# Kernel tuning notes

Measured on AMD Instinct MI355X. Metric: run time of the kernel, lower is better.

## Reference

```python
import jax, jax.numpy as jnp
import numpy as np

E = 8        # n_experts
H = 1024     # hidden_size == input_size
M = 2048     # intermediate_size
K = 2        # topk
SE = 1       # share_expert
BSZ, SEQ = 2, 1024
W_SCALE = 0.02


def setup_inputs() -> dict:
    key = jax.random.key(0)
    ks = jax.random.split(key, 9)
    return {
        "x": jax.random.normal(ks[0], (BSZ, SEQ, H), jnp.float32),
        "gate_w": jax.random.normal(ks[1], (E, H), jnp.float32) * W_SCALE,
        "beta": jnp.zeros((E,), jnp.float32),
        "gate_proj_w": jax.random.normal(ks[2], (E, H, M), jnp.float32) * W_SCALE,
        "up_proj_w": jax.random.normal(ks[3], (E, H, M), jnp.float32) * W_SCALE,
        "down_proj_w": jax.random.normal(ks[4], (E, M, H), jnp.float32) * W_SCALE,
        "shared_gate_w": jax.random.normal(ks[5], (SE, H, M), jnp.float32) * W_SCALE,
        "shared_up_w": jax.random.normal(ks[6], (SE, H, M), jnp.float32) * W_SCALE,
        "shared_down_w": jax.random.normal(ks[7], (SE, M, H), jnp.float32) * W_SCALE,
    }


def reference(x, gate_w, beta, gate_proj_w, up_proj_w, down_proj_w,
              shared_gate_w, shared_up_w, shared_down_w):
    B0, S0, H0 = x.shape
    xt = x.reshape(-1, H0)                       # [B, H], B = B0*S0 tokens
    B = xt.shape[0]

    # --- routing: top-k on (logits + beta), gate prob = sigmoid(selected logits) ---
    logits = xt @ gate_w.T                       # [B, E]
    _, idx = jax.lax.top_k(logits + beta, K)     # [B, K] expert indices
    probs = jax.nn.sigmoid(jnp.take_along_axis(logits, idx, axis=-1))  # [B, K]

    # combine weights c[b, e]: scatter top-k probs (equivalent to index_add combine)
    c = jnp.zeros((B, E), xt.dtype).at[jnp.arange(B)[:, None], idx].add(probs)

    # --- per-expert SwiGLU over all tokens, then weighted combine by c ---
    g = jnp.einsum('bh,ehm->bem', xt, gate_proj_w)   # [B, E, M]
    u = jnp.einsum('bh,ehm->bem', xt, up_proj_w)     # [B, E, M]
    h = jax.nn.silu(g) * u                           # [B, E, M]
    eo = jnp.einsum('bem,emh->beh', h, down_proj_w)  # [B, E, H]
    combined = jnp.einsum('beh,be->bh', eo, c)       # [B, H]

    # --- shared expert(s): applied to every token, no gating ---
    sg = jnp.einsum('bh,ehm->bem', xt, shared_gate_w)
    su = jnp.einsum('bh,ehm->bem', xt, shared_up_w)
    sh = jax.nn.silu(sg) * su
    shared_out = jnp.einsum('bem,emh->beh', sh, shared_down_w).sum(axis=1)  # [B, H]

    return (combined + shared_out).reshape(B0, S0, H0)
```

## Files before the change

kernel.cpp:

```cpp
#include <hip/hip_runtime.h>

#define NE 8
#define HD 1024
#define MD 2048
#define NT 2048
#define NSH 4224

typedef __attribute__((ext_vector_type(8))) short s16x8;
typedef __attribute__((ext_vector_type(4))) float f32x4;
typedef __attribute__((ext_vector_type(8))) unsigned short u16x8;
typedef __attribute__((ext_vector_type(4))) unsigned short u16x4;

__device__ __forceinline__ unsigned short f2bf(float f) {
    union { float f; unsigned int i; } v; v.f = f;
    unsigned int u = v.i;
    return (unsigned short)((u + 0x7FFFu + ((u >> 16) & 1u)) >> 16);
}
__device__ __forceinline__ float bf2f(unsigned short u) {
    union { unsigned int i; float f; } v; v.i = ((unsigned int)u) << 16; return v.f;
}

__device__ __forceinline__ void gld16(const unsigned short* g, short* l) {
    __builtin_amdgcn_global_load_lds(
        (const __attribute__((address_space(1))) unsigned int*)g,
        (__attribute__((address_space(3))) unsigned int*)l,
        16, 0, 0);
}


__global__ __launch_bounds__(256) void k_cvt(
    const float* __restrict__ s, unsigned short* __restrict__ d, int n)
{
    int i = (blockIdx.x * 256 + threadIdx.x) * 4;
    int stride = gridDim.x * 256 * 4;
    for (; i < n; i += stride) {
        float4 v = *(const float4*)(s + i);
        u16x4 o;
        o[0] = f2bf(v.x); o[1] = f2bf(v.y); o[2] = f2bf(v.z); o[3] = f2bf(v.w);
        *(u16x4*)(d + i) = o;
    }
}

__global__ __launch_bounds__(256) void k_cvt_gu(
    const float* __restrict__ wg, const float* __restrict__ wu,
    const float* __restrict__ swg, const float* __restrict__ swu,
    unsigned short* __restrict__ o)
{
    int e = blockIdx.z;
    const float* sg = (e < NE) ? wg + (size_t)e * HD * MD : swg;
    const float* su = (e < NE) ? wu + (size_t)e * HD * MD : swu;
    unsigned short* dst = o + (size_t)e * (2 * MD) * HD;
    int k0 = blockIdx.x * 64, n0s = blockIdx.y * 32;
    __shared__ float T[64 * 67];
    int tid = threadIdx.x;
    #pragma unroll
    for (int p = 0; p < 4; p++) {
        int idx = p * 256 + tid;
        int row = idx >> 4, f4 = idx & 15;
        const float* s = (f4 < 8) ? sg : su;
        int n4 = (f4 & 7) * 4;
        float4 v = *(const float4*)(s + (size_t)(k0 + row) * MD + n0s + n4);
        *(float4*)(&T[row * 67 + (f4 >> 3) * 32 + n4]) = v;
    }
    __syncthreads();
    const int KC = HD / 8;
    #pragma unroll
    for (int p = 0; p < 2; p++) {
        int cid = p * 256 + tid;
        int g = cid >> 7, rem = cid & 127;
        int kc = rem >> 4, ni = rem & 15;
        int colT = (ni & 1) * 32 + ((g * 16 + ni) >> 1);
        u16x8 r;
        #pragma unroll
        for (int j = 0; j < 8; j++) r[j] = f2bf(T[(kc * 8 + j) * 67 + colT]);
        size_t oidx = ((size_t)((n0s >> 3) + g) * KC + (k0 >> 3) + kc) * 128 + ni * 8;
        *(u16x8*)(dst + oidx) = r;
    }
}

__global__ __launch_bounds__(256) void k_cvt_d(
    const float* __restrict__ wr, const float* __restrict__ wsd,
    unsigned short* __restrict__ o)
{
    int e = blockIdx.z;
    const float* src = (e < NE) ? wr + (size_t)e * MD * HD : wsd;
    unsigned short* dst = o + (size_t)e * MD * HD;
    int k0 = blockIdx.x * 64, n0 = blockIdx.y * 64;
    __shared__ float T[64 * 67];
    int tid = threadIdx.x;
    #pragma unroll
    for (int p = 0; p < 4; p++) {
        int idx = p * 256 + tid;
        int row = idx >> 4, n4 = (idx & 15) * 4;
        float4 v = *(const float4*)(src + (size_t)(k0 + row) * HD + n0 + n4);
        *(float4*)(&T[row * 67 + n4]) = v;
    }
    __syncthreads();
    const int KC = MD / 8;
    #pragma unroll
    for (int p = 0; p < 2; p++) {
        int cid = p * 256 + tid;
        int g = cid >> 7, rem = cid & 127;
        int kc = rem >> 4, ni = rem & 15;
        u16x8 r;
        #pragma unroll
        for (int j = 0; j < 8; j++) r[j] = f2bf(T[(kc * 8 + j) * 67 + g * 16 + ni]);
        size_t oidx = ((size_t)((n0 >> 4) + g) * KC + (k0 >> 3) + kc) * 128 + ni * 8;
        *(u16x8*)(dst + oidx) = r;
    }
}

__global__ __launch_bounds__(256) void k_route(
    const float* __restrict__ x, const float* __restrict__ gw,
    const float* __restrict__ beta,
    int* __restrict__ cnt, int* __restrict__ list, int* __restrict__ slot,
    float* __restrict__ rprob)
{
    int wave = threadIdx.x >> 6, lane = threadIdx.x & 63;
    int t = blockIdx.x * 4 + wave;
    const float4* xp = (const float4*)(x + (size_t)t * HD) + lane * 4;
    float4 xv[4];
    #pragma unroll
    for (int j = 0; j < 4; j++) xv[j] = xp[j];

    float logit[NE];
    #pragma unroll
    for (int e = 0; e < NE; e++) {
        const float4* gp = (const float4*)(gw + e * HD) + lane * 4;
        float s = 0.f;
        #pragma unroll
        for (int j = 0; j < 4; j++) {
            float4 g = gp[j];
            s += xv[j].x * g.x + xv[j].y * g.y + xv[j].z * g.z + xv[j].w * g.w;
        }
        for (int off = 32; off > 0; off >>= 1) s += __shfl_xor(s, off);
        logit[e] = s;
    }
    if (lane == 0) {
        float v[NE];
        #pragma unroll
        for (int e = 0; e < NE; e++) v[e] = logit[e] + beta[e];
        int i1 = 0; float m1 = v[0];
        #pragma unroll
        for (int e = 1; e < NE; e++) if (v[e] > m1) { m1 = v[e]; i1 = e; }
        int i2 = -1; float m2 = -3.4e38f;
        #pragma unroll
        for (int e = 0; e < NE; e++) if (e != i1 && v[e] > m2) { m2 = v[e]; i2 = e; }
        if (i2 < 0) i2 = (i1 + 1) & 7;
        float p1 = 1.f / (1.f + __expf(-logit[i1]));
        float p2 = 1.f / (1.f + __expf(-logit[i2]));
        int pos1 = atomicAdd(cnt + i1, 1);
        list[i1 * NT + pos1] = t; slot[t * 2 + 0] = (i1 << 16) | pos1; rprob[t * 2 + 0] = p1;
        int pos2 = atomicAdd(cnt + i2, 1);
        list[i2 * NT + pos2] = t; slot[t * 2 + 1] = (i2 << 16) | pos2; rprob[t * 2 + 1] = p2;
    }
}

__global__ void k_scan(const int* __restrict__ cnt, int* __restrict__ base) {
    if (threadIdx.x == 0) {
        int run = 0;
        for (int e = 0; e < NE; e++) { base[e] = run; run += (cnt[e] + 15) & ~15; }
        base[NE] = run;
    }
}

__global__ __launch_bounds__(256, 4) void k_gateup(
    const unsigned short* __restrict__ x,
    const unsigned short* __restrict__ wgu,
    const int* __restrict__ cnt, const int* __restrict__ base, const int* __restrict__ list,
    unsigned short* __restrict__ h)
{
    int e = blockIdx.z;
    int i0 = blockIdx.y * 128;
    int n0 = blockIdx.x * 128;
    int cnte = (e < NE) ? cnt[e] : NT;
    if (i0 >= cnte) return;
    int rbase = (e < NE) ? base[e] : NSH;
    const unsigned short* wb = wgu + (size_t)e * (2 * MD) * HD;

    __shared__ short As[2][128 * 32];
    __shared__ short Bs[2][8 * 512];
    __shared__ int tok[128];

    int tid = threadIdx.x;
    int lane = tid & 63, wave = tid >> 6;
    if (tid < 128) {
        int gi = i0 + tid;
        tok[tid] = (e < NE) ? ((gi < cnte) ? list[e * NT + gi] : list[e * NT]) : gi;
    }
    __syncthreads();

    int rr = wave * 32 + (lane >> 2);
    int kc = ((lane & 3) ^ ((lane >> 3) & 3)) * 8;
    size_t gaA0 = (size_t)tok[rr] * HD + kc;
    size_t gaA1 = (size_t)tok[rr + 16] * HD + kc;
    const int KC = HD / 8;
    size_t gaB0 = ((size_t)((n0 >> 4) + 2 * wave) * KC) * 128 + lane * 8;
    size_t gaB1 = gaB0 + (size_t)KC * 128;
    int loA0 = (wave * 32) * 32, loA1 = (wave * 32 + 16) * 32;
    int loB0 = (2 * wave) * 512, loB1 = (2 * wave + 1) * 512;

    int wr = (wave >> 1) * 64, wc = (wave & 1) * 64;
    int m = lane & 15, q = lane >> 4;
    int sa = (m >> 1) & 3;

    f32x4 acc[4][4];
    #pragma unroll
    for (int a = 0; a < 4; a++)
        #pragma unroll
        for (int b = 0; b < 4; b++) acc[a][b] = (f32x4)0.f;

    gld16(x + gaA0, &As[0][loA0]);
    gld16(x + gaA1, &As[0][loA1]);
    gld16(wb + gaB0, &Bs[0][loB0]);
    gld16(wb + gaB1, &Bs[0][loB1]);

    int it = 0;
    for (int k0 = 0; k0 < HD; k0 += 32, it ^= 1) {
        __syncthreads();
        int nk = k0 + 32;
        if (nk < HD) {
            int nb = it ^ 1;
            gld16(x + gaA0 + nk, &As[nb][loA0]);
            gld16(x + gaA1 + nk, &As[nb][loA1]);
            gld16(wb + gaB0 + (size_t)nk * 16, &Bs[nb][loB0]);
            gld16(wb + gaB1 + (size_t)nk * 16, &Bs[nb][loB1]);
        }
        s16x8 af[4];
        #pragma unroll
        for (int ti = 0; ti < 4; ti++)
            af[ti] = *(const s16x8*)(&As[it][(wr + ti * 16 + m) * 32 + (q ^ sa) * 8]);
        #pragma unroll
        for (int tj = 0; tj < 4; tj++) {
            s16x8 bf = *(const s16x8*)(&Bs[it][((wave & 1) * 4 + tj) * 512 + q * 128 + m * 8]);
            #pragma unroll
            for (int ti = 0; ti < 4; ti++)
                acc[ti][tj] = __builtin_amdgcn_mfma_f32_16x16x32_bf16(af[ti], bf, acc[ti][tj], 0, 0, 0);
        }
    }
    #pragma unroll
    for (int ti = 0; ti < 4; ti++)
        #pragma unroll
        for (int tj = 0; tj < 4; tj++)
            #pragma unroll
            for (int r = 0; r < 4; r++) {
                float v = acc[ti][tj][r];
                float uo = __shfl_xor(v, 1);
                int gi = i0 + wr + ti * 16 + q * 4 + r;
                if (!(m & 1) && gi < cnte) {
                    float g = v;
                    float hv = (g / (1.f + __expf(-g))) * uo;
                    int col = (n0 + wc + tj * 16 + m) >> 1;
                    int rw = rbase + gi;
                    size_t hi = ((size_t)(rw >> 4) * (MD >> 3) + (col >> 3)) * 128
                              + (rw & 15) * 8 + (col & 7);
                    h[hi] = f2bf(hv);
                }
            }
}

__global__ __launch_bounds__(256, 4) void k_down(
    const unsigned short* __restrict__ wd_all,
    const int* __restrict__ cnt, const int* __restrict__ base,
    const unsigned short* __restrict__ h, unsigned short* __restrict__ eo)
{
    int e = blockIdx.z;
    int i0 = blockIdx.y * 128;
    int n0 = blockIdx.x * 128;
    int cnte = (e < NE) ? cnt[e] : NT;
    if (i0 >= cnte) return;
    int rbase = (e < NE) ? base[e] : NSH;
    const unsigned short* wd = wd_all + (size_t)e * MD * HD;

    __shared__ short As[2][8 * 512];
    __shared__ short Bd[2][8 * 512];

    int tid = threadIdx.x;
    int lane = tid & 63, wave = tid >> 6;
    int r0 = rbase + i0;
    const int KC = MD / 8;
    size_t gaA0 = ((size_t)((r0 >> 4) + 2 * wave) * KC) * 128 + lane * 8;
    size_t gaA1 = gaA0 + (size_t)KC * 128;
    size_t gaB0 = ((size_t)((n0 >> 4) + 2 * wave) * KC) * 128 + lane * 8;
    size_t gaB1 = gaB0 + (size_t)KC * 128;
    int lo0 = (2 * wave) * 512, lo1 = (2 * wave + 1) * 512;

    int wr = (wave >> 1) * 64, wc = (wave & 1) * 64;
    int m = lane & 15, q = lane >> 4;

    f32x4 acc[4][4];
    #pragma unroll
    for (int a = 0; a < 4; a++)
        #pragma unroll
        for (int b = 0; b < 4; b++) acc[a][b] = (f32x4)0.f;

    gld16(h + gaA0, &As[0][lo0]);
    gld16(h + gaA1, &As[0][lo1]);
    gld16(wd + gaB0, &Bd[0][lo0]);
    gld16(wd + gaB1, &Bd[0][lo1]);

    int it = 0;
    for (int k0 = 0; k0 < MD; k0 += 32, it ^= 1) {
        __syncthreads();
        int nk = k0 + 32;
        if (nk < MD) {
            int nb = it ^ 1;
            gld16(h + gaA0 + (size_t)nk * 16, &As[nb][lo0]);
            gld16(h + gaA1 + (size_t)nk * 16, &As[nb][lo1]);
            gld16(wd + gaB0 + (size_t)nk * 16, &Bd[nb][lo0]);
            gld16(wd + gaB1 + (size_t)nk * 16, &Bd[nb][lo1]);
        }
        s16x8 af[4];
        #pragma unroll
        for (int ti = 0; ti < 4; ti++)
            af[ti] = *(const s16x8*)(&As[it][((wave >> 1) * 4 + ti) * 512 + q * 128 + m * 8]);
        #pragma unroll
        for (int tj = 0; tj < 4; tj++) {
            s16x8 bd = *(const s16x8*)(&Bd[it][((wave & 1) * 4 + tj) * 512 + q * 128 + m * 8]);
            #pragma unroll
            for (int ti = 0; ti < 4; ti++)
                acc[ti][tj] = __builtin_amdgcn_mfma_f32_16x16x32_bf16(af[ti], bd, acc[ti][tj], 0, 0, 0);
        }
    }
    #pragma unroll
    for (int ti = 0; ti < 4; ti++)
        #pragma unroll
        for (int tj = 0; tj < 4; tj++)
            #pragma unroll
            for (int r = 0; r < 4; r++) {
                int gi = i0 + wr + ti * 16 + q * 4 + r;
                if (gi < cnte) {
                    int col = n0 + wc + tj * 16 + m;
                    eo[(size_t)(rbase + gi) * HD + col] = f2bf(acc[ti][tj][r]);
                }
            }
}

__global__ __launch_bounds__(256) void k_combine(
    const unsigned short* __restrict__ eo, const int* __restrict__ slot,
    const float* __restrict__ rprob, const int* __restrict__ base,
    float* __restrict__ out)
{
    int t = blockIdx.x;
    int s0 = slot[t * 2], s1 = slot[t * 2 + 1];
    float p0 = rprob[t * 2], p1 = rprob[t * 2 + 1];
    int r0 = base[s0 >> 16] + (s0 & 0xFFFF);
    int r1 = base[s1 >> 16] + (s1 & 0xFFFF);
    int rs = NSH + t;
    int c = threadIdx.x * 4;
    u16x4 a = *(const u16x4*)(eo + (size_t)r0 * HD + c);
    u16x4 b = *(const u16x4*)(eo + (size_t)r1 * HD + c);
    u16x4 s = *(const u16x4*)(eo + (size_t)rs * HD + c);
    float4 res;
    res.x = p0 * bf2f(a[0]) + p1 * bf2f(b[0]) + bf2f(s[0]);
    res.y = p0 * bf2f(a[1]) + p1 * bf2f(b[1]) + bf2f(s[1]);
    res.z = p0 * bf2f(a[2]) + p1 * bf2f(b[2]) + bf2f(s[2]);
    res.w = p0 * bf2f(a[3]) + p1 * bf2f(b[3]) + bf2f(s[3]);
    *(float4*)(out + (size_t)t * HD + c) = res;
}

extern "C" void kernel_launch(void* const* d_in, const int* in_sizes, int n_in,
                              void* d_out, int out_size, void* d_ws, size_t ws_size,
                              hipStream_t stream)
{
    const float* x    = (const float*)d_in[0];
    const float* gw   = (const float*)d_in[1];
    const float* beta = (const float*)d_in[2];
    const float* wg   = (const float*)d_in[3];
    const float* wu   = (const float*)d_in[4];
    const float* wd   = (const float*)d_in[5];
    const float* swg  = (const float*)d_in[6];
    const float* swu  = (const float*)d_in[7];
    const float* swd  = (const float*)d_in[8];
    float* out = (float*)d_out;

    char* ws = (char*)d_ws;
    const size_t MB = (size_t)1 << 20;
    int*   cnt   = (int*)(ws + 0);
    int*   basep = (int*)(ws + 64);
    int*   list  = (int*)(ws + 1024);
    int*   slot  = (int*)(ws + 1024 + 65536);
    float* rprob = (float*)(ws + 1024 + 65536 + 16384);
    unsigned short* xb   = (unsigned short*)(ws + 1 * MB);
    unsigned short* eo   = (unsigned short*)(ws + 6 * MB);
    unsigned short* wgut = (unsigned short*)(ws + 20 * MB);
    unsigned short* wdt  = (unsigned short*)(ws + 92 * MB);
    unsigned short* h    = (unsigned short*)(ws + 128 * MB);

    hipMemsetAsync(ws, 0, 128, stream);

    const int NX = NT * HD;
    k_cvt<<<512, 256, 0, stream>>>(x, xb, NX);

    dim3 tgu(HD / 64, MD / 32, NE + 1);
    k_cvt_gu<<<tgu, 256, 0, stream>>>(wg, wu, swg, swu, wgut);
    dim3 td(MD / 64, HD / 64, NE + 1);
    k_cvt_d<<<td, 256, 0, stream>>>(wd, swd, wdt);

    k_route<<<NT / 4, 256, 0, stream>>>(x, gw, beta, cnt, list, slot, rprob);
    k_scan<<<1, 64, 0, stream>>>(cnt, basep);

    dim3 g3(2 * MD / 128, NT / 128, NE + 1);
    k_gateup<<<g3, 256, 0, stream>>>(xb, wgut, cnt, basep, list, h);

    dim3 g4(HD / 128, NT / 128, NE + 1);
    k_down<<<g4, 256, 0, stream>>>(wdt, cnt, basep, h, eo);

    k_combine<<<NT, 256, 0, stream>>>(eo, slot, rprob, basep, out);
}
```

Baseline: 450.9 us.

## Compact MoE tile scheduling, fuse x conversion into routing, retile weight converters

The x-to-bf16 conversion moves into the routing kernel, which removes one kernel launch and one read of x. The scan kernel now builds a compact list of live (expert, row-tile) pairs, so the gate/up and down GEMMs launch a 1D grid with an XCD-style swizzle instead of a 3D grid where many blocks exit early. The weight conversion kernels use 32x128 tiles with a 132-float LDS pitch for wider coalesced reads, and occupancy bounds rise to 5 blocks. The costs are a serial tile-map loop in the single-thread scan and the risk that the higher occupancy bound causes register spills.

```diff
diff --git a/kernel.cpp b/kernel.cpp
--- a/kernel.cpp
+++ b/kernel.cpp
@@ -28,19 +28,6 @@
 }
 
 
-__global__ __launch_bounds__(256) void k_cvt(
-    const float* __restrict__ s, unsigned short* __restrict__ d, int n)
-{
-    int i = (blockIdx.x * 256 + threadIdx.x) * 4;
-    int stride = gridDim.x * 256 * 4;
-    for (; i < n; i += stride) {
-        float4 v = *(const float4*)(s + i);
-        u16x4 o;
-        o[0] = f2bf(v.x); o[1] = f2bf(v.y); o[2] = f2bf(v.z); o[3] = f2bf(v.w);
-        *(u16x4*)(d + i) = o;
-    }
-}
-
 __global__ __launch_bounds__(256) void k_cvt_gu(
     const float* __restrict__ wg, const float* __restrict__ wu,
     const float* __restrict__ swg, const float* __restrict__ swu,
@@ -50,30 +37,30 @@
     const float* sg = (e < NE) ? wg + (size_t)e * HD * MD : swg;
     const float* su = (e < NE) ? wu + (size_t)e * HD * MD : swu;
     unsigned short* dst = o + (size_t)e * (2 * MD) * HD;
-    int k0 = blockIdx.x * 64, n0s = blockIdx.y * 32;
-    __shared__ float T[64 * 67];
+    int k0 = blockIdx.x * 32, n0 = blockIdx.y * 128;
+    __shared__ float T[2 * 32 * 132];
     int tid = threadIdx.x;
     #pragma unroll
     for (int p = 0; p < 4; p++) {
         int idx = p * 256 + tid;
-        int row = idx >> 4, f4 = idx & 15;
-        const float* s = (f4 < 8) ? sg : su;
-        int n4 = (f4 & 7) * 4;
-        float4 v = *(const float4*)(s + (size_t)(k0 + row) * MD + n0s + n4);
-        *(float4*)(&T[row * 67 + (f4 >> 3) * 32 + n4]) = v;
+        int row = idx >> 5, l4 = (idx & 31) * 4;
+        float4 vg = *(const float4*)(sg + (size_t)(k0 + row) * MD + n0 + l4);
+        float4 vu = *(const float4*)(su + (size_t)(k0 + row) * MD + n0 + l4);
+        *(float4*)(&T[row * 132 + l4]) = vg;
+        *(float4*)(&T[32 * 132 + row * 132 + l4]) = vu;
     }
     __syncthreads();
     const int KC = HD / 8;
     #pragma unroll
-    for (int p = 0; p < 2; p++) {
-        int cid = p * 256 + tid;
-        int g = cid >> 7, rem = cid & 127;
-        int kc = rem >> 4, ni = rem & 15;
-        int colT = (ni & 1) * 32 + ((g * 16 + ni) >> 1);
+    for (int p = 0; p < 4; p++) {
+        int c = p * 256 + tid;
+        int ni = c & 15, ns = (c >> 4) & 15, kc = c >> 8;
+        int colL = ns * 8 + (ni >> 1);
+        const float* Tm = &T[(ni & 1) * 32 * 132];
         u16x8 r;
         #pragma unroll
-        for (int j = 0; j < 8; j++) r[j] = f2bf(T[(kc * 8 + j) * 67 + colT]);
-        size_t oidx = ((size_t)((n0s >> 3) + g) * KC + (k0 >> 3) + kc) * 128 + ni * 8;
+        for (int j = 0; j < 8; j++) r[j] = f2bf(Tm[(kc * 8 + j) * 132 + colL]);
+        size_t oidx = ((size_t)((n0 >> 3) + ns) * KC + (k0 >> 3) + kc) * 128 + ni * 8;
         *(u16x8*)(dst + oidx) = r;
     }
 }
@@ -85,27 +72,27 @@
     int e = blockIdx.z;
     const float* src = (e < NE) ? wr + (size_t)e * MD * HD : wsd;
     unsigned short* dst = o + (size_t)e * MD * HD;
-    int k0 = blockIdx.x * 64, n0 = blockIdx.y * 64;
-    __shared__ float T[64 * 67];
+    int k0 = blockIdx.x * 32, n0 = blockIdx.y * 128;
+    __shared__ float T[32 * 132];
     int tid = threadIdx.x;
     #pragma unroll
     for (int p = 0; p < 4; p++) {
         int idx = p * 256 + tid;
-        int row = idx >> 4, n4 = (idx & 15) * 4;
-        float4 v = *(const float4*)(src + (size_t)(k0 + row) * HD + n0 + n4);
-        *(float4*)(&T[row * 67 + n4]) = v;
+        int row = idx >> 5, l4 = (idx & 31) * 4;
+        float4 v = *(const float4*)(src + (size_t)(k0 + row) * HD + n0 + l4);
+        *(float4*)(&T[row * 132 + l4]) = v;
     }
     __syncthreads();
     const int KC = MD / 8;
     #pragma unroll
     for (int p = 0; p < 2; p++) {
-        int cid = p * 256 + tid;
-        int g = cid >> 7, rem = cid & 127;
-        int kc = rem >> 4, ni = rem & 15;
+        int c = p * 256 + tid;
+        int ni = c & 15, ns = (c >> 4) & 7, kc = c >> 7;
+        int colL = ns * 16 + ni;
         u16x8 r;
         #pragma unroll
-        for (int j = 0; j < 8; j++) r[j] = f2bf(T[(kc * 8 + j) * 67 + g * 16 + ni]);
-        size_t oidx = ((size_t)((n0 >> 4) + g) * KC + (k0 >> 3) + kc) * 128 + ni * 8;
+        for (int j = 0; j < 8; j++) r[j] = f2bf(T[(kc * 8 + j) * 132 + colL]);
+        size_t oidx = ((size_t)((n0 >> 4) + ns) * KC + (k0 >> 3) + kc) * 128 + ni * 8;
         *(u16x8*)(dst + oidx) = r;
     }
 }
@@ -114,7 +101,7 @@
     const float* __restrict__ x, const float* __restrict__ gw,
     const float* __restrict__ beta,
     int* __restrict__ cnt, int* __restrict__ list, int* __restrict__ slot,
-    float* __restrict__ rprob)
+    float* __restrict__ rprob, unsigned short* __restrict__ xb)
 {
     int wave = threadIdx.x >> 6, lane = threadIdx.x & 63;
     int t = blockIdx.x * 4 + wave;
@@ -122,6 +109,14 @@
     float4 xv[4];
     #pragma unroll
     for (int j = 0; j < 4; j++) xv[j] = xp[j];
+
+    u16x8 o0, o1;
+    o0[0] = f2bf(xv[0].x); o0[1] = f2bf(xv[0].y); o0[2] = f2bf(xv[0].z); o0[3] = f2bf(xv[0].w);
+    o0[4] = f2bf(xv[1].x); o0[5] = f2bf(xv[1].y); o0[6] = f2bf(xv[1].z); o0[7] = f2bf(xv[1].w);
+    o1[0] = f2bf(xv[2].x); o1[1] = f2bf(xv[2].y); o1[2] = f2bf(xv[2].z); o1[3] = f2bf(xv[2].w);
+    o1[4] = f2bf(xv[3].x); o1[5] = f2bf(xv[3].y); o1[6] = f2bf(xv[3].z); o1[7] = f2bf(xv[3].w);
+    *(u16x8*)(xb + (size_t)t * HD + lane * 16) = o0;
+    *(u16x8*)(xb + (size_t)t * HD + lane * 16 + 8) = o1;
 
     float logit[NE];
     #pragma unroll
@@ -156,44 +151,58 @@
     }
 }
 
-__global__ void k_scan(const int* __restrict__ cnt, int* __restrict__ base) {
+__global__ void k_scan(const int* __restrict__ cnt, int* __restrict__ base,
+                       int* __restrict__ tmap, int* __restrict__ ntile) {
     if (threadIdx.x == 0) {
-        int run = 0;
-        for (int e = 0; e < NE; e++) { base[e] = run; run += (cnt[e] + 15) & ~15; }
+        int run = 0, nt = 0;
+        for (int e = 0; e < NE; e++) {
+            base[e] = run;
+            int c = cnt[e];
+            run += (c + 15) & ~15;
+            for (int i0 = 0; i0 < c; i0 += 128) tmap[nt++] = (e << 8) | (i0 >> 7);
+        }
         base[NE] = run;
-    }
-}
-
-__global__ __launch_bounds__(256, 4) void k_gateup(
+        for (int i0 = 0; i0 < NT; i0 += 128) tmap[nt++] = (NE << 8) | (i0 >> 7);
+        *ntile = nt;
+    }
+}
+
+__global__ __launch_bounds__(256, 5) void k_gateup(
     const unsigned short* __restrict__ x,
     const unsigned short* __restrict__ wgu,
     const int* __restrict__ cnt, const int* __restrict__ base, const int* __restrict__ list,
+    const int* __restrict__ tmap, const int* __restrict__ ntile,
     unsigned short* __restrict__ h)
 {
-    int e = blockIdx.z;
-    int i0 = blockIdx.y * 128;
-    int n0 = blockIdx.x * 128;
+    int bid = blockIdx.x;
+    int swz = (bid & 7) * 224 + (bid >> 3);
+    int ti = swz >> 5, ntl = swz & 31;
+    if (ti >= *ntile) return;
+    int mv = tmap[ti];
+    int e = mv >> 8;
+    int i0 = (mv & 255) << 7;
+    int n0 = ntl * 128;
     int cnte = (e < NE) ? cnt[e] : NT;
-    if (i0 >= cnte) return;
     int rbase = (e < NE) ? base[e] : NSH;
     const unsigned short* wb = wgu + (size_t)e * (2 * MD) * HD;
 
     __shared__ short As[2][128 * 32];
     __shared__ short Bs[2][8 * 512];
-    __shared__ int tok[128];
 
     int tid = threadIdx.x;
     int lane = tid & 63, wave = tid >> 6;
-    if (tid < 128) {
-        int gi = i0 + tid;
-        tok[tid] = (e < NE) ? ((gi < cnte) ? list[e * NT + gi] : list[e * NT]) : gi;
-    }
-    __syncthreads();
 
     int rr = wave * 32 + (lane >> 2);
+    int gi0r = i0 + rr, gi1r = i0 + rr + 16;
+    int t0, t1;
+    if (e < NE) {
+        t0 = list[e * NT + (gi0r < cnte ? gi0r : cnte - 1)];
+        t1 = list[e * NT + (gi1r < cnte ? gi1r : cnte - 1)];
+    } else { t0 = gi0r; t1 = gi1r; }
+
     int kc = ((lane & 3) ^ ((lane >> 3) & 3)) * 8;
-    size_t gaA0 = (size_t)tok[rr] * HD + kc;
-    size_t gaA1 = (size_t)tok[rr + 16] * HD + kc;
+    size_t gaA0 = (size_t)t0 * HD + kc;
+    size_t gaA1 = (size_t)t1 * HD + kc;
     const int KC = HD / 8;
     size_t gaB0 = ((size_t)((n0 >> 4) + 2 * wave) * KC) * 128 + lane * 8;
     size_t gaB1 = gaB0 + (size_t)KC * 128;
@@ -228,25 +237,25 @@
         }
         s16x8 af[4];
         #pragma unroll
-        for (int ti = 0; ti < 4; ti++)
-            af[ti] = *(const s16x8*)(&As[it][(wr + ti * 16 + m) * 32 + (q ^ sa) * 8]);
+        for (int ti2 = 0; ti2 < 4; ti2++)
+            af[ti2] = *(const s16x8*)(&As[it][(wr + ti2 * 16 + m) * 32 + (q ^ sa) * 8]);
         #pragma unroll
         for (int tj = 0; tj < 4; tj++) {
             s16x8 bf = *(const s16x8*)(&Bs[it][((wave & 1) * 4 + tj) * 512 + q * 128 + m * 8]);
             #pragma unroll
-            for (int ti = 0; ti < 4; ti++)
-                acc[ti][tj] = __builtin_amdgcn_mfma_f32_16x16x32_bf16(af[ti], bf, acc[ti][tj], 0, 0, 0);
-        }
-    }
-    #pragma unroll
-    for (int ti = 0; ti < 4; ti++)
+            for (int ti2 = 0; ti2 < 4; ti2++)
+                acc[ti2][tj] = __builtin_amdgcn_mfma_f32_16x16x32_bf16(af[ti2], bf, acc[ti2][tj], 0, 0, 0);
+        }
+    }
+    #pragma unroll
+    for (int ti2 = 0; ti2 < 4; ti2++)
         #pragma unroll
         for (int tj = 0; tj < 4; tj++)
             #pragma unroll
             for (int r = 0; r < 4; r++) {
-                float v = acc[ti][tj][r];
+                float v = acc[ti2][tj][r];
                 float uo = __shfl_xor(v, 1);
-                int gi = i0 + wr + ti * 16 + q * 4 + r;
+                int gi = i0 + wr + ti2 * 16 + q * 4 + r;
                 if (!(m & 1) && gi < cnte) {
                     float g = v;
                     float hv = (g / (1.f + __expf(-g))) * uo;
@@ -259,16 +268,21 @@
             }
 }
 
-__global__ __launch_bounds__(256, 4) void k_down(
+__global__ __launch_bounds__(256, 5) void k_down(
     const unsigned short* __restrict__ wd_all,
     const int* __restrict__ cnt, const int* __restrict__ base,
+    const int* __restrict__ tmap, const int* __restrict__ ntile,
     const unsigned short* __restrict__ h, unsigned short* __restrict__ eo)
 {
-    int e = blockIdx.z;
-    int i0 = blockIdx.y * 128;
-    int n0 = blockIdx.x * 128;
+    int bid = blockIdx.x;
+    int swz = (bid & 7) * 56 + (bid >> 3);
+    int ti = swz >> 3, ntl = swz & 7;
+    if (ti >= *ntile) return;
+    int mv = tmap[ti];
+    int e = mv >> 8;
+    int i0 = (mv & 255) << 7;
+    int n0 = ntl * 128;
     int cnte = (e < NE) ? cnt[e] : NT;
-    if (i0 >= cnte) return;
     int rbase = (e < NE) ? base[e] : NSH;
     const unsigned short* wd = wd_all + (size_t)e * MD * HD;
 
@@ -312,26 +326,26 @@
         }
         s16x8 af[4];
         #pragma unroll
-        for (int ti = 0; ti < 4; ti++)
-            af[ti] = *(const s16x8*)(&As[it][((wave >> 1) * 4 + ti) * 512 + q * 128 + m * 8]);
+        for (int ti2 = 0; ti2 < 4; ti2++)
+            af[ti2] = *(const s16x8*)(&As[it][((wave >> 1) * 4 + ti2) * 512 + q * 128 + m * 8]);
         #pragma unroll
         for (int tj = 0; tj < 4; tj++) {
             s16x8 bd = *(const s16x8*)(&Bd[it][((wave & 1) * 4 + tj) * 512 + q * 128 + m * 8]);
             #pragma unroll
-            for (int ti = 0; ti < 4; ti++)
-                acc[ti][tj] = __builtin_amdgcn_mfma_f32_16x16x32_bf16(af[ti], bd, acc[ti][tj], 0, 0, 0);
-        }
-    }
-    #pragma unroll
-    for (int ti = 0; ti < 4; ti++)
+            for (int ti2 = 0; ti2 < 4; ti2++)
+                acc[ti2][tj] = __builtin_amdgcn_mfma_f32_16x16x32_bf16(af[ti2], bd, acc[ti2][tj], 0, 0, 0);
+        }
+    }
+    #pragma unroll
+    for (int ti2 = 0; ti2 < 4; ti2++)
         #pragma unroll
         for (int tj = 0; tj < 4; tj++)
             #pragma unroll
             for (int r = 0; r < 4; r++) {
-                int gi = i0 + wr + ti * 16 + q * 4 + r;
+                int gi = i0 + wr + ti2 * 16 + q * 4 + r;
                 if (gi < cnte) {
                     int col = n0 + wc + tj * 16 + m;
-                    eo[(size_t)(rbase + gi) * HD + col] = f2bf(acc[ti][tj][r]);
+                    eo[(size_t)(rbase + gi) * HD + col] = f2bf(acc[ti2][tj][r]);
                 }
             }
 }
@@ -378,6 +392,8 @@
     const size_t MB = (size_t)1 << 20;
     int*   cnt   = (int*)(ws + 0);
     int*   basep = (int*)(ws + 64);
+    int*   ntile = (int*)(ws + 128);
+    int*   tmap  = (int*)(ws + 192);
     int*   list  = (int*)(ws + 1024);
     int*   slot  = (int*)(ws + 1024 + 65536);
     float* rprob = (float*)(ws + 1024 + 65536 + 16384);
@@ -389,22 +405,17 @@
 
     hipMemsetAsync(ws, 0, 128, stream);
 
-    const int NX = NT * HD;
-    k_cvt<<<512, 256, 0, stream>>>(x, xb, NX);
-
-    dim3 tgu(HD / 64, MD / 32, NE + 1);
+    dim3 tgu(HD / 32, MD / 128, NE + 1);
     k_cvt_gu<<<tgu, 256, 0, stream>>>(wg, wu, swg, swu, wgut);
-    dim3 td(MD / 64, HD / 64, NE + 1);
+    dim3 td(MD / 32, HD / 128, NE + 1);
     k_cvt_d<<<td, 256, 0, stream>>>(wd, swd, wdt);
 
-    k_route<<<NT / 4, 256, 0, stream>>>(x, gw, beta, cnt, list, slot, rprob);
-    k_scan<<<1, 64, 0, stream>>>(cnt, basep);
-
-    dim3 g3(2 * MD / 128, NT / 128, NE + 1);
-    k_gateup<<<g3, 256, 0, stream>>>(xb, wgut, cnt, basep, list, h);
-
-    dim3 g4(HD / 128, NT / 128, NE + 1);
-    k_down<<<g4, 256, 0, stream>>>(wdt, cnt, basep, h, eo);
+    k_route<<<NT / 4, 256, 0, stream>>>(x, gw, beta, cnt, list, slot, rprob, xb);
+    k_scan<<<1, 64, 0, stream>>>(cnt, basep, tmap, ntile);
+
+    k_gateup<<<1792, 256, 0, stream>>>(xb, wgut, cnt, basep, list, tmap, ntile, h);
+
+    k_down<<<448, 256, 0, stream>>>(wdt, cnt, basep, tmap, ntile, h, eo);
 
     k_combine<<<NT, 256, 0, stream>>>(eo, slot, rprob, basep, out);
 }
```

Result: slower. 505.2 us (+12.0%).
